# Kernel tuning notes

Hardware: AMD Instinct MI355X
Metric: run time of the kernel (lower is better)

The kernel has to match this reference:

```python
import jax, jax.numpy as jnp
import numpy as np

B, T, S, H, NH, F = 16, 512, 512, 1024, 16, 4096
HD = H // NH


def _mha(x, bias, mem, wq, bq, wk, bk, wv, bv, wo, bo):
    # THUMT MultiHeadAttention: q scaled by head_dim**-0.5, additive bias on logits
    b, t, h = x.shape
    q = (x @ wq + bq) * (HD ** -0.5)
    k = mem @ wk + bk
    v = mem @ wv + bv
    split = lambda z: z.reshape(z.shape[0], z.shape[1], NH, HD).transpose(0, 2, 1, 3)
    logits = jnp.einsum('bhqd,bhkd->bhqk', split(q), split(k)) + bias
    w = jax.nn.softmax(logits, axis=-1)
    o = jnp.einsum('bhqk,bhkd->bhqd', w, split(v))
    o = o.transpose(0, 2, 1, 3).reshape(b, t, h)
    return o @ wo + bo


def _lstm(inp, w, b):
    # inp: [B, T, 2H]; gates affine over concat([x_t, h], -1): [3H] -> [4H]
    bsz = inp.shape[0]
    def step(carry, xt):
        c, hdd = carry
        g = jnp.concatenate([xt, hdd], axis=-1) @ w + b
        i, j, f, o = jnp.split(g, 4, axis=-1)
        new_c = jax.nn.sigmoid(f) * c + jax.nn.sigmoid(i) * jnp.tanh(j)
        new_h = jax.nn.sigmoid(o) * jnp.tanh(new_c)
        return (new_c, new_h), new_h
    init = (jnp.zeros((bsz, H), inp.dtype), jnp.zeros((bsz, H), inp.dtype))
    _, hs = jax.lax.scan(step, init, inp.transpose(1, 0, 2))  # [T,B,H]
    return hs.transpose(1, 0, 2)


def setup_inputs() -> dict:
    key = jax.random.key(0)
    ks = jax.random.split(key, 16)
    d = {}
    d['x'] = jax.random.normal(ks[0], (B, T, H), jnp.float32)
    d['memory'] = jax.random.normal(ks[1], (B, S, H), jnp.float32)
    d['src_bias'] = jnp.zeros((B, 1, 1, S), jnp.float32)
    causal = jnp.triu(jnp.full((T, T), -1e9, jnp.float32), k=1)
    d['tgt_bias'] = causal[None, None]
    sc = 0.02
    names = ['src_wq', 'src_wk', 'src_wv', 'src_wo', 'tgt_wq', 'tgt_wk', 'tgt_wv', 'tgt_wo']
    for i, n in enumerate(names):
        d[n] = jax.random.normal(ks[2 + i], (H, H), jnp.float32) * sc
        d[n.replace('w', 'b')] = jnp.zeros((H,), jnp.float32)
    d['lstm_w'] = jax.random.normal(ks[10], (3 * H, 4 * H), jnp.float32) * sc
    d['lstm_b'] = jnp.zeros((4 * H,), jnp.float32)
    d['ffn_w1'] = jax.random.normal(ks[11], (H, F), jnp.float32) * sc
    d['ffn_b1'] = jnp.zeros((F,), jnp.float32)
    d['ffn_w2'] = jax.random.normal(ks[12], (F, H), jnp.float32) * sc
    d['ffn_b2'] = jnp.zeros((H,), jnp.float32)
    return d


def reference(x, memory, src_bias, tgt_bias,
              src_wq, src_bq, src_wk, src_bk, src_wv, src_bv, src_wo, src_bo,
              tgt_wq, tgt_bq, tgt_wk, tgt_bk, tgt_wv, tgt_bv, tgt_wo, tgt_bo,
              lstm_w, lstm_b, ffn_w1, ffn_b1, ffn_w2, ffn_b2):
    c_src = _mha(x, src_bias, memory, src_wq, src_bq, src_wk, src_bk, src_wv, src_bv, src_wo, src_bo)
    c_tgt = _mha(x, tgt_bias, x, tgt_wq, tgt_bq, tgt_wk, tgt_bk, tgt_wv, tgt_bv, tgt_wo, tgt_bo)
    c = c_src + c_tgt  # comb_mode='sum'
    hiddens = _lstm(jnp.concatenate([x, c], axis=-1), lstm_w, lstm_b)
    hiddens = jax.nn.relu(hiddens @ ffn_w1 + ffn_b1) @ ffn_w2 + ffn_b2  # FeedForward
    return hiddens  # dropout is identity in eval
```

## Files before the change

### kernel.cpp

```cpp
#include <hip/hip_runtime.h>
#include <hip/hip_bf16.h>
#include <stdint.h>


typedef unsigned short u16;
typedef unsigned int u32;
typedef unsigned long long u64;
typedef __bf16 bf16x8 __attribute__((ext_vector_type(8)));
typedef float f32x4 __attribute__((ext_vector_type(4)));
typedef int int32x4 __attribute__((ext_vector_type(4)));
typedef unsigned long long u64x2 __attribute__((ext_vector_type(2)));

#define DEV static __device__ __forceinline__

DEV u16 f2bf(float x) {
  u32 u = __builtin_bit_cast(u32, x);
  u += 0x7FFF + ((u >> 16) & 1);
  return (u16)(u >> 16);
}

DEV bf16x8 ldfrag(const void* p) {
  int32x4 v = *(const int32x4*)p;
  return __builtin_bit_cast(bf16x8, v);
}

DEV bf16x8 mkfrag(u64 lo, u64 hi) {
  u64x2 v;
  v.x = lo;
  v.y = hi;
  return __builtin_bit_cast(bf16x8, v);
}

DEV f32x4 mfma_bf16(bf16x8 a, bf16x8 b, f32x4 c) {
  return __builtin_amdgcn_mfma_f32_16x16x32_bf16(a, b, c, 0, 0, 0);
}

DEV void load_lds16(const u16* g, u16* l) {
  __builtin_amdgcn_global_load_lds(
      (__attribute__((address_space(1))) void*)(uintptr_t)g,
      (__attribute__((address_space(3))) void*)(uintptr_t)l, 16, 0, 0);
}


__global__ __launch_bounds__(256) void cvt_bf16_kernel(u16* __restrict__ out,
                                                       const float* __restrict__ in,
                                                       int n4) {
  int i = blockIdx.x * 256 + threadIdx.x;
  if (i >= n4) return;
  float4 v = ((const float4*)in)[i];
  ushort4 s;
  s.x = f2bf(v.x); s.y = f2bf(v.y); s.z = f2bf(v.z); s.w = f2bf(v.w);
  ((ushort4*)out)[i] = s;
}

__global__ __launch_bounds__(256) void cvt_x_kernel(u16* __restrict__ out,
                                                    const float* __restrict__ in) {
  int i = blockIdx.x * 256 + threadIdx.x;
  int r = i >> 8, cg4 = i & 255;
  float4 v = ((const float4*)in)[i];
  ushort4 s;
  s.x = f2bf(v.x); s.y = f2bf(v.y); s.z = f2bf(v.z); s.w = f2bf(v.w);
  *(ushort4*)(out + (size_t)r * 2048 + cg4 * 4) = s;
}

__global__ __launch_bounds__(256) void convt_kernel(u16* __restrict__ out,
                                                    const float* __restrict__ in,
                                                    int K, int N, int koff, float scale) {
  __shared__ float tile[32][33];
  const int tid = threadIdx.x;
  const int n0 = blockIdx.x * 32, k0 = blockIdx.y * 32;
  const int c = tid & 31, r = tid >> 5;
#pragma unroll
  for (int i = 0; i < 4; ++i)
    tile[r + i * 8][c] = in[(size_t)(k0 + r + i * 8 + koff) * N + n0 + c];
  __syncthreads();
#pragma unroll
  for (int i = 0; i < 4; ++i)
    out[(size_t)(n0 + r + i * 8) * K + k0 + c] = f2bf(tile[c][r + i * 8] * scale);
}

__global__ __launch_bounds__(256) void convt_perm_kernel(u16* __restrict__ out,
                                                         const float* __restrict__ in,
                                                         int K, int koff) {
  __shared__ float tile[32][33];
  const int tid = threadIdx.x;
  const int u0 = blockIdx.x * 32, k0 = blockIdx.y * 32, g = blockIdx.z;
  const int c = tid & 31, r = tid >> 5;
#pragma unroll
  for (int i = 0; i < 4; ++i)
    tile[r + i * 8][c] = in[(size_t)(k0 + r + i * 8 + koff) * 4096 + g * 1024 + u0 + c];
  __syncthreads();
#pragma unroll
  for (int i = 0; i < 4; ++i)
    out[(size_t)((u0 + r + i * 8) * 4 + g) * K + k0 + c] = f2bf(tile[c][r + i * 8]);
}

__global__ __launch_bounds__(256) void pack_bias_kernel(float* __restrict__ out,
                                                        const float* __restrict__ in) {
  int p = blockIdx.x * 256 + threadIdx.x;
  out[p] = in[(p & 3) * 1024 + (p >> 2)];
}

template <int OUTBF, int ACCUM, int RELU, int PERM>
__global__ __launch_bounds__(256) void gemm_bt_kernel(
    const u16* __restrict__ A, int lda, const u16* __restrict__ Bt,
    const float* __restrict__ bias, float bscale,
    void* __restrict__ outp, int ostride,
    const float* __restrict__ cacc, int cstride, int K) {
  __shared__ u16 As[128 * 32];
  __shared__ u16 Bs[128 * 32];
  const int tid = threadIdx.x;
  const int wave = tid >> 6, lane = tid & 63;
  const int lr = lane & 15, lg = lane >> 4;
  const int m0 = blockIdx.y * 128, n0 = blockIdx.x * 128;
  const int wr = (wave >> 1) * 64, wc = (wave & 1) * 64;

  f32x4 acc[4][4] = {};

  const int sr = lane >> 2, sce = (lane & 3) * 8;
  const u16* gA = A + (size_t)(m0 + wave * 16 + sr) * lda + sce;
  const u16* gB = Bt + (size_t)(n0 + wave * 16 + sr) * K + sce;
  u16* lA = As + wave * 16 * 32;
  u16* lB = Bs + wave * 16 * 32;

  for (int k0 = 0; k0 < K; k0 += 32) {
    __syncthreads();
    load_lds16(gA + k0, lA);
    load_lds16(gA + k0 + (size_t)64 * lda, lA + 64 * 32);
    load_lds16(gB + k0, lB);
    load_lds16(gB + k0 + (size_t)64 * K, lB + 64 * 32);
    __syncthreads();
    bf16x8 af[4], bfr[4];
    const u16* pa = As + (wr + lr) * 32 + lg * 8;
    const u16* pb = Bs + (wc + lr) * 32 + lg * 8;
#pragma unroll
    for (int i = 0; i < 4; ++i) af[i] = ldfrag(pa + i * 16 * 32);
#pragma unroll
    for (int j = 0; j < 4; ++j) bfr[j] = ldfrag(pb + j * 16 * 32);
#pragma unroll
    for (int i = 0; i < 4; ++i)
#pragma unroll
      for (int j = 0; j < 4; ++j)
        acc[i][j] = mfma_bf16(af[i], bfr[j], acc[i][j]);
  }

  const int col0 = n0 + wc + lr;
  const int row0 = m0 + wr + lg * 4;
#pragma unroll
  for (int i = 0; i < 4; ++i) {
#pragma unroll
    for (int j = 0; j < 4; ++j) {
      const int c = col0 + j * 16;
      const float bv = bias ? bias[c] * bscale : 0.f;
#pragma unroll
      for (int ii = 0; ii < 4; ++ii) {
        const int r = row0 + i * 16 + ii;
        float v = acc[i][j][ii] + bv;
        if (ACCUM) v += cacc[(size_t)r * cstride + c];
        if (RELU) v = fmaxf(v, 0.f);
        const int rp = (PERM == 2) ? ((r & 15) * 512 + (r >> 4)) : r;
        if (OUTBF) ((u16*)outp)[(size_t)rp * ostride + c] = f2bf(v);
        else       ((float*)outp)[(size_t)rp * ostride + c] = v;
      }
    }
  }
}

template <int CAUSAL>
__global__ __launch_bounds__(256) void flash_kernel(
    const u16* __restrict__ Q, const u16* __restrict__ Kb, const u16* __restrict__ Vb,
    const float* __restrict__ sbias, u16* __restrict__ O) {
  __shared__ u16 Kl[64 * 72];
  __shared__ u16 Vt[64 * 72];
  __shared__ u16 Pl[64 * 72];
  const int tid = threadIdx.x, wave = tid >> 6, lane = tid & 63;
  const int lr = lane & 15, lg = lane >> 4;
  const int q0 = blockIdx.x * 64, hh = blockIdx.y, b = blockIdx.z;

  bf16x8 qf[2];
  {
    const u16* qp = Q + (size_t)(b * 512 + q0 + wave * 16 + lr) * 1024 + hh * 64 + lg * 8;
    qf[0] = ldfrag(qp);
    qf[1] = ldfrag(qp + 32);
  }
  f32x4 oacc[4] = {};
  float mrun[4], lsum[4];
#pragma unroll
  for (int ii = 0; ii < 4; ++ii) { mrun[ii] = -3e38f; lsum[ii] = 0.f; }

  const int ntiles = CAUSAL ? (q0 / 64 + 1) : 8;
  for (int ti = 0; ti < ntiles; ++ti) {
    const int s0 = ti * 64;
    {
      const int r = tid >> 2, ch = (tid & 3) * 16;
      const u16* kp = Kb + (size_t)(b * 512 + s0 + r) * 1024 + hh * 64 + ch;
      const u16* vp = Vb + (size_t)(b * 512 + s0 + r) * 1024 + hh * 64 + ch;
      int32x4 k0v = *(const int32x4*)kp;
      int32x4 k1v = *(const int32x4*)(kp + 8);
      int32x4 v0v = *(const int32x4*)vp;
      int32x4 v1v = *(const int32x4*)(vp + 8);
      *(int32x4*)&Kl[r * 72 + ch] = k0v;
      *(int32x4*)&Kl[r * 72 + ch + 8] = k1v;
      const u16* v0p = (const u16*)&v0v;
      const u16* v1p = (const u16*)&v1v;
#pragma unroll
      for (int j = 0; j < 8; ++j) {
        Vt[(ch + j) * 72 + r] = v0p[j];
        Vt[(ch + 8 + j) * 72 + r] = v1p[j];
      }
    }
    __syncthreads();
    f32x4 sf[4] = {};
#pragma unroll
    for (int j = 0; j < 4; ++j)
#pragma unroll
      for (int ks = 0; ks < 2; ++ks) {
        bf16x8 kf = ldfrag(&Kl[(j * 16 + lr) * 72 + ks * 32 + lg * 8]);
        sf[j] = mfma_bf16(qf[ks], kf, sf[j]);
      }
    if (!CAUSAL) {
#pragma unroll
      for (int j = 0; j < 4; ++j) {
        const float bv = sbias[b * 512 + s0 + j * 16 + lr];
#pragma unroll
        for (int ii = 0; ii < 4; ++ii) sf[j][ii] += bv;
      }
    } else {
#pragma unroll
      for (int j = 0; j < 4; ++j) {
        const int s = s0 + j * 16 + lr;
#pragma unroll
        for (int ii = 0; ii < 4; ++ii) {
          const int q = q0 + wave * 16 + lg * 4 + ii;
          if (s > q) sf[j][ii] -= 1e9f;
        }
      }
    }
    float sc[4], rs[4];
#pragma unroll
    for (int ii = 0; ii < 4; ++ii) {
      float m = fmaxf(fmaxf(sf[0][ii], sf[1][ii]), fmaxf(sf[2][ii], sf[3][ii]));
#pragma unroll
      for (int off = 1; off < 16; off <<= 1) m = fmaxf(m, __shfl_xor(m, off));
      const float mn = fmaxf(mrun[ii], m);
      sc[ii] = __expf(mrun[ii] - mn);
      mrun[ii] = mn;
      rs[ii] = 0.f;
    }
#pragma unroll
    for (int j = 0; j < 4; ++j)
#pragma unroll
      for (int ii = 0; ii < 4; ++ii) {
        const float p = __expf(sf[j][ii] - mrun[ii]);
        rs[ii] += p;
        Pl[(wave * 16 + lg * 4 + ii) * 72 + j * 16 + lr] = f2bf(p);
      }
#pragma unroll
    for (int ii = 0; ii < 4; ++ii) {
      float r = rs[ii];
#pragma unroll
      for (int off = 1; off < 16; off <<= 1) r += __shfl_xor(r, off);
      lsum[ii] = lsum[ii] * sc[ii] + r;
    }
#pragma unroll
    for (int df = 0; df < 4; ++df)
#pragma unroll
      for (int ii = 0; ii < 4; ++ii) oacc[df][ii] *= sc[ii];
    __syncthreads();
    bf16x8 pf[2];
    pf[0] = ldfrag(&Pl[(wave * 16 + lr) * 72 + lg * 8]);
    pf[1] = ldfrag(&Pl[(wave * 16 + lr) * 72 + 32 + lg * 8]);
#pragma unroll
    for (int df = 0; df < 4; ++df)
#pragma unroll
      for (int ks = 0; ks < 2; ++ks) {
        bf16x8 vf = ldfrag(&Vt[(df * 16 + lr) * 72 + ks * 32 + lg * 8]);
        oacc[df] = mfma_bf16(pf[ks], vf, oacc[df]);
      }
    __syncthreads();
  }
#pragma unroll
  for (int df = 0; df < 4; ++df)
#pragma unroll
    for (int ii = 0; ii < 4; ++ii) {
      const float v = oacc[df][ii] / lsum[ii];
      O[(size_t)(b * 512 + q0 + wave * 16 + lg * 4 + ii) * 1024 + hh * 64 + df * 16 + lr] =
          f2bf(v);
    }
}

#define SCAN_NW 32
__global__ __launch_bounds__(256, 1) void lstm_scan_kernel(
    const u16* __restrict__ Whp, const float* __restrict__ gx,
    u16* __restrict__ hbuf) {
  const int tid = threadIdx.x, wave = tid >> 6, lane = tid & 63;
  const int lr = lane & 15, lg = lane >> 4;
  const int g = blockIdx.x;
  __shared__ float part[2][4][16][128];
  const int gb = tid >> 4;
  const int up = tid & 15;
  float cs0 = 0.f, cs1 = 0.f;
  const u64 SENT = 0xFFFFFFFFFFFFFFFFull;

  const u16* wbase = Whp + (size_t)(g * 128 + lr) * 1024 + wave * 256 + lg * 8;
  const float* gxp = gx + (size_t)gb * 512 * 4096 + g * 128 + up * 8;

  for (int t = 0; t < 512; ++t) {
    const float4 gxv0 = *(const float4*)(gxp + (size_t)t * 4096);
    const float4 gxv1 = *(const float4*)(gxp + (size_t)t * 4096 + 4);
    const u16* hp = hbuf + (size_t)t * 16384 + lr * 1024 + wave * 256 + lg * 8;
    u64 hw[16];
#pragma unroll
    for (int kc = 0; kc < 8; ++kc) {
      hw[kc * 2] = __hip_atomic_load((const u64*)(hp + kc * 32),
                                     __ATOMIC_RELAXED, __HIP_MEMORY_SCOPE_AGENT);
      hw[kc * 2 + 1] = __hip_atomic_load((const u64*)(hp + kc * 32 + 4),
                                         __ATOMIC_RELAXED, __HIP_MEMORY_SCOPE_AGENT);
    }
    {
      int guard = 0;
      for (;;) {
        bool ok = true;
#pragma unroll
        for (int i = 0; i < 16; ++i) ok &= (hw[i] != SENT);
        if (__all((int)ok)) break;
        __builtin_amdgcn_s_sleep(4);
        if (++guard > (1 << 20)) break;
#pragma unroll
        for (int kc = 0; kc < 8; ++kc) {
          if (hw[kc * 2] == SENT)
            hw[kc * 2] = __hip_atomic_load((const u64*)(hp + kc * 32),
                                           __ATOMIC_RELAXED, __HIP_MEMORY_SCOPE_AGENT);
          if (hw[kc * 2 + 1] == SENT)
            hw[kc * 2 + 1] = __hip_atomic_load((const u64*)(hp + kc * 32 + 4),
                                               __ATOMIC_RELAXED, __HIP_MEMORY_SCOPE_AGENT);
        }
      }
    }
    f32x4 acc[8] = {};
#pragma unroll
    for (int kc = 0; kc < 8; ++kc) {
      const bf16x8 hf = mkfrag(hw[kc * 2], hw[kc * 2 + 1]);
#pragma unroll
      for (int j = 0; j < 8; ++j)
        acc[j] = mfma_bf16(hf, ldfrag(wbase + j * 16 * 1024 + kc * 32), acc[j]);
    }
    const int p = t & 1;
#pragma unroll
    for (int j = 0; j < 8; ++j)
#pragma unroll
      for (int ii = 0; ii < 4; ++ii)
        part[p][wave][lg * 4 + ii][j * 16 + lr] = acc[j][ii];
    __syncthreads();
    float s[8];
#pragma unroll
    for (int k = 0; k < 8; ++k)
      s[k] = part[p][0][gb][up * 8 + k] + part[p][1][gb][up * 8 + k] +
             part[p][2][gb][up * 8 + k] + part[p][3][gb][up * 8 + k];
    float hA, hB;
    {
      const float si = s[0] + gxv0.x, sj = s[1] + gxv0.y;
      const float sf_ = s[2] + gxv0.z, so = s[3] + gxv0.w;
      const float ig = 1.f / (1.f + __expf(-si));
      const float jg = 1.f - 2.f / (__expf(2.f * sj) + 1.f);
      const float fg = 1.f / (1.f + __expf(-sf_));
      const float og = 1.f / (1.f + __expf(-so));
      cs0 = fg * cs0 + ig * jg;
      hA = og * (1.f - 2.f / (__expf(2.f * cs0) + 1.f));
    }
    {
      const float si = s[4] + gxv1.x, sj = s[5] + gxv1.y;
      const float sf_ = s[6] + gxv1.z, so = s[7] + gxv1.w;
      const float ig = 1.f / (1.f + __expf(-si));
      const float jg = 1.f - 2.f / (__expf(2.f * sj) + 1.f);
      const float fg = 1.f / (1.f + __expf(-sf_));
      const float og = 1.f / (1.f + __expf(-so));
      cs1 = fg * cs1 + ig * jg;
      hB = og * (1.f - 2.f / (__expf(2.f * cs1) + 1.f));
    }
    const u32 myw = (u32)f2bf(hA) | ((u32)f2bf(hB) << 16);
    const u32 otherw = (u32)__shfl_down((int)myw, 1);
    if (!(up & 1)) {
      u64 w64 = (u64)myw | ((u64)otherw << 32);
      u64* dst = (u64*)(hbuf + (size_t)(t + 1) * 16384 + gb * 1024 + g * 32 + up * 2);
      __hip_atomic_store(dst, w64, __ATOMIC_RELAXED, __HIP_MEMORY_SCOPE_AGENT);
    }
  }
}


extern "C" void kernel_launch(void* const* d_in, const int* in_sizes, int n_in,
                              void* d_out, int out_size, void* d_ws, size_t ws_size,
                              hipStream_t stream) {
  const float* x        = (const float*)d_in[0];
  const float* mem      = (const float*)d_in[1];
  const float* src_bias = (const float*)d_in[2];
  const float* w_src_q = (const float*)d_in[4];  const float* b_src_q = (const float*)d_in[5];
  const float* w_src_k = (const float*)d_in[6];  const float* b_src_k = (const float*)d_in[7];
  const float* w_src_v = (const float*)d_in[8];  const float* b_src_v = (const float*)d_in[9];
  const float* w_src_o = (const float*)d_in[10]; const float* b_src_o = (const float*)d_in[11];
  const float* w_tgt_q = (const float*)d_in[12]; const float* b_tgt_q = (const float*)d_in[13];
  const float* w_tgt_k = (const float*)d_in[14]; const float* b_tgt_k = (const float*)d_in[15];
  const float* w_tgt_v = (const float*)d_in[16]; const float* b_tgt_v = (const float*)d_in[17];
  const float* w_tgt_o = (const float*)d_in[18]; const float* b_tgt_o = (const float*)d_in[19];
  const float* lstm_w  = (const float*)d_in[20]; const float* lstm_b  = (const float*)d_in[21];
  const float* w1 = (const float*)d_in[22]; const float* b1f = (const float*)d_in[23];
  const float* w2 = (const float*)d_in[24]; const float* b2f = (const float*)d_in[25];

  char* ws = (char*)d_ws;
  const size_t MiB = 1024ull * 1024ull;
  u16*   xcb  = (u16*)(ws + 0);
  u16*   wlp  = (u16*)(ws + 32 * MiB);
  u16*   whp  = (u16*)(ws + 48 * MiB);
  u16*   w1t  = (u16*)(ws + 56 * MiB);
  u16*   w2t  = (u16*)(ws + 64 * MiB);
  float* pb   = (float*)(ws + 72 * MiB);
  u16*   hbuf = (u16*)(ws + 73 * MiB);
  u16*   memb = (u16*)(ws + 90 * MiB);
  u16*   wt[8];
  for (int i = 0; i < 8; ++i) wt[i] = (u16*)(ws + 106 * MiB + (size_t)i * 2 * MiB);
  u16*   bq   = (u16*)(ws + 122 * MiB);
  u16*   bk   = (u16*)(ws + 138 * MiB);
  u16*   bv   = (u16*)(ws + 154 * MiB);
  u16*   ao_s = (u16*)(ws + 170 * MiB);
  u16*   ao_t = (u16*)(ws + 186 * MiB);
  float* c32  = (float*)(ws + 202 * MiB);
  float* gx   = (float*)(ws + 90 * MiB);
  u16*   ffn1 = (u16*)(ws + 90 * MiB);

  hipMemsetAsync(hbuf + 16384, 0xFF, (size_t)512 * 16384 * 2, stream);
  hipMemsetAsync(hbuf, 0, 32768, stream);

  cvt_x_kernel<<<8192, 256, 0, stream>>>(xcb, x);
  cvt_bf16_kernel<<<8192, 256, 0, stream>>>(memb, mem, 2097152);
  const dim3 g1k(32, 32);
  convt_kernel<<<g1k, 256, 0, stream>>>(wt[0], w_src_q, 1024, 1024, 0, 0.125f);
  convt_kernel<<<g1k, 256, 0, stream>>>(wt[1], w_src_k, 1024, 1024, 0, 1.f);
  convt_kernel<<<g1k, 256, 0, stream>>>(wt[2], w_src_v, 1024, 1024, 0, 1.f);
  convt_kernel<<<g1k, 256, 0, stream>>>(wt[3], w_src_o, 1024, 1024, 0, 1.f);
  convt_kernel<<<g1k, 256, 0, stream>>>(wt[4], w_tgt_q, 1024, 1024, 0, 0.125f);
  convt_kernel<<<g1k, 256, 0, stream>>>(wt[5], w_tgt_k, 1024, 1024, 0, 1.f);
  convt_kernel<<<g1k, 256, 0, stream>>>(wt[6], w_tgt_v, 1024, 1024, 0, 1.f);
  convt_kernel<<<g1k, 256, 0, stream>>>(wt[7], w_tgt_o, 1024, 1024, 0, 1.f);
  convt_perm_kernel<<<dim3(32, 64, 4), 256, 0, stream>>>(wlp, lstm_w, 2048, 0);
  convt_perm_kernel<<<dim3(32, 32, 4), 256, 0, stream>>>(whp, lstm_w, 1024, 2048);
  convt_kernel<<<dim3(128, 32), 256, 0, stream>>>(w1t, w1, 1024, 4096, 0, 1.f);
  convt_kernel<<<dim3(32, 128), 256, 0, stream>>>(w2t, w2, 4096, 1024, 0, 1.f);
  pack_bias_kernel<<<16, 256, 0, stream>>>(pb, lstm_b);

  const dim3 gN1(8, 64);
  const dim3 gN4(32, 64);

  gemm_bt_kernel<1, 0, 0, 0><<<gN1, 256, 0, stream>>>(xcb, 2048, wt[0], b_src_q, 0.125f, bq, 1024, nullptr, 0, 1024);
  gemm_bt_kernel<1, 0, 0, 0><<<gN1, 256, 0, stream>>>(memb, 1024, wt[1], b_src_k, 1.f, bk, 1024, nullptr, 0, 1024);
  gemm_bt_kernel<1, 0, 0, 0><<<gN1, 256, 0, stream>>>(memb, 1024, wt[2], b_src_v, 1.f, bv, 1024, nullptr, 0, 1024);
  flash_kernel<0><<<dim3(8, 16, 16), 256, 0, stream>>>(bq, bk, bv, src_bias, ao_s);
  gemm_bt_kernel<1, 0, 0, 0><<<gN1, 256, 0, stream>>>(xcb, 2048, wt[4], b_tgt_q, 0.125f, bq, 1024, nullptr, 0, 1024);
  gemm_bt_kernel<1, 0, 0, 0><<<gN1, 256, 0, stream>>>(xcb, 2048, wt[5], b_tgt_k, 1.f, bk, 1024, nullptr, 0, 1024);
  gemm_bt_kernel<1, 0, 0, 0><<<gN1, 256, 0, stream>>>(xcb, 2048, wt[6], b_tgt_v, 1.f, bv, 1024, nullptr, 0, 1024);
  flash_kernel<1><<<dim3(8, 16, 16), 256, 0, stream>>>(bq, bk, bv, nullptr, ao_t);
  gemm_bt_kernel<0, 0, 0, 0><<<gN1, 256, 0, stream>>>(ao_s, 1024, wt[3], b_src_o, 1.f, c32, 1024, nullptr, 0, 1024);
  gemm_bt_kernel<1, 1, 0, 0><<<gN1, 256, 0, stream>>>(ao_t, 1024, wt[7], b_tgt_o, 1.f, xcb + 1024, 2048, c32, 1024, 1024);
  gemm_bt_kernel<0, 0, 0, 0><<<gN4, 256, 0, stream>>>(xcb, 2048, wlp, pb, 1.f, gx, 4096, nullptr, 0, 2048);
  lstm_scan_kernel<<<dim3(SCAN_NW), 256, 0, stream>>>(whp, gx, hbuf);
  gemm_bt_kernel<1, 0, 1, 0><<<gN4, 256, 0, stream>>>(hbuf + 16384, 1024, w1t, b1f, 1.f, ffn1, 4096, nullptr, 0, 1024);
  gemm_bt_kernel<0, 0, 0, 2><<<gN1, 256, 0, stream>>>(ffn1, 4096, w2t, b2f, 1.f, (float*)d_out, 1024, nullptr, 0, 4096);
}
```

Before: 3.002 ms.

## Fuse QKV projection GEMMs, swizzle GEMM tile order, pad LSTM LDS partials

Merges the separate target Q/K/V projection GEMMs into one wide GEMM producing an interleaved [rows, 3072] buffer. It does the same for the source K/V pair into [rows, 2048], using the fact that the transposed weights sit back to back in the workspace. Biases are packed by a new small kernel, and the flash kernel takes row strides so it can read the interleaved buffers. It also remaps workgroup IDs in the GEMM so tiles sharing operands run together, and pads the LSTM scan's shared partial-sum array to cut bank conflicts. The aim is fewer launches, better operand reuse and fewer LDS conflicts. The risk is that the fused GEMM depends on the implicit contiguous weight layout.

```diff
diff --git a/kernel.cpp b/kernel.cpp
--- a/kernel.cpp
+++ b/kernel.cpp
@@ -33,6 +33,10 @@
 
 DEV f32x4 mfma_bf16(bf16x8 a, bf16x8 b, f32x4 c) {
   return __builtin_amdgcn_mfma_f32_16x16x32_bf16(a, b, c, 0, 0, 0);
+}
+
+DEV u64 aload(const u64* p) {
+  return __hip_atomic_load(p, __ATOMIC_RELAXED, __HIP_MEMORY_SCOPE_AGENT);
 }
 
 DEV void load_lds16(const u16* g, u16* l) {
@@ -99,6 +103,14 @@
                                                         const float* __restrict__ in) {
   int p = blockIdx.x * 256 + threadIdx.x;
   out[p] = in[(p & 3) * 1024 + (p >> 2)];
+}
+
+__global__ __launch_bounds__(256) void pack_bias3_kernel(
+    float* __restrict__ out, const float* __restrict__ b0,
+    const float* __restrict__ b1, const float* __restrict__ b2, float s0) {
+  int p = blockIdx.x * 256 + threadIdx.x;
+  float v = (p < 1024) ? b0[p] * s0 : (p < 2048 ? b1[p - 1024] : b2[p - 2048]);
+  out[p] = v;
 }
 
 template <int OUTBF, int ACCUM, int RELU, int PERM>
@@ -112,7 +124,10 @@
   const int tid = threadIdx.x;
   const int wave = tid >> 6, lane = tid & 63;
   const int lr = lane & 15, lg = lane >> 4;
-  const int m0 = blockIdx.y * 128, n0 = blockIdx.x * 128;
+  const int nwg = gridDim.x * gridDim.y;
+  const int wgid = blockIdx.y * gridDim.x + blockIdx.x;
+  const int swz = (wgid & 7) * (nwg >> 3) + (wgid >> 3);
+  const int m0 = (swz / gridDim.x) * 128, n0 = (swz % gridDim.x) * 128;
   const int wr = (wave >> 1) * 64, wc = (wave & 1) * 64;
 
   f32x4 acc[4][4] = {};
@@ -169,7 +184,7 @@
 template <int CAUSAL>
 __global__ __launch_bounds__(256) void flash_kernel(
     const u16* __restrict__ Q, const u16* __restrict__ Kb, const u16* __restrict__ Vb,
-    const float* __restrict__ sbias, u16* __restrict__ O) {
+    const float* __restrict__ sbias, u16* __restrict__ O, int qs, int ks) {
   __shared__ u16 Kl[64 * 72];
   __shared__ u16 Vt[64 * 72];
   __shared__ u16 Pl[64 * 72];
@@ -179,7 +194,7 @@
 
   bf16x8 qf[2];
   {
-    const u16* qp = Q + (size_t)(b * 512 + q0 + wave * 16 + lr) * 1024 + hh * 64 + lg * 8;
+    const u16* qp = Q + (size_t)(b * 512 + q0 + wave * 16 + lr) * qs + hh * 64 + lg * 8;
     qf[0] = ldfrag(qp);
     qf[1] = ldfrag(qp + 32);
   }
@@ -193,8 +208,8 @@
     const int s0 = ti * 64;
     {
       const int r = tid >> 2, ch = (tid & 3) * 16;
-      const u16* kp = Kb + (size_t)(b * 512 + s0 + r) * 1024 + hh * 64 + ch;
-      const u16* vp = Vb + (size_t)(b * 512 + s0 + r) * 1024 + hh * 64 + ch;
+      const u16* kp = Kb + (size_t)(b * 512 + s0 + r) * ks + hh * 64 + ch;
+      const u16* vp = Vb + (size_t)(b * 512 + s0 + r) * ks + hh * 64 + ch;
       int32x4 k0v = *(const int32x4*)kp;
       int32x4 k1v = *(const int32x4*)(kp + 8);
       int32x4 v0v = *(const int32x4*)vp;
@@ -214,9 +229,9 @@
 #pragma unroll
     for (int j = 0; j < 4; ++j)
 #pragma unroll
-      for (int ks = 0; ks < 2; ++ks) {
-        bf16x8 kf = ldfrag(&Kl[(j * 16 + lr) * 72 + ks * 32 + lg * 8]);
-        sf[j] = mfma_bf16(qf[ks], kf, sf[j]);
+      for (int ks2 = 0; ks2 < 2; ++ks2) {
+        bf16x8 kf = ldfrag(&Kl[(j * 16 + lr) * 72 + ks2 * 32 + lg * 8]);
+        sf[j] = mfma_bf16(qf[ks2], kf, sf[j]);
       }
     if (!CAUSAL) {
 #pragma unroll
@@ -273,9 +288,9 @@
 #pragma unroll
     for (int df = 0; df < 4; ++df)
 #pragma unroll
-      for (int ks = 0; ks < 2; ++ks) {
-        bf16x8 vf = ldfrag(&Vt[(df * 16 + lr) * 72 + ks * 32 + lg * 8]);
-        oacc[df] = mfma_bf16(pf[ks], vf, oacc[df]);
+      for (int ks2 = 0; ks2 < 2; ++ks2) {
+        bf16x8 vf = ldfrag(&Vt[(df * 16 + lr) * 72 + ks2 * 32 + lg * 8]);
+        oacc[df] = mfma_bf16(pf[ks2], vf, oacc[df]);
       }
     __syncthreads();
   }
@@ -296,7 +311,7 @@
   const int tid = threadIdx.x, wave = tid >> 6, lane = tid & 63;
   const int lr = lane & 15, lg = lane >> 4;
   const int g = blockIdx.x;
-  __shared__ float part[2][4][16][128];
+  __shared__ float part[2][4][16][132];
   const int gb = tid >> 4;
   const int up = tid & 15;
   float cs0 = 0.f, cs1 = 0.f;
@@ -304,18 +319,17 @@
 
   const u16* wbase = Whp + (size_t)(g * 128 + lr) * 1024 + wave * 256 + lg * 8;
   const float* gxp = gx + (size_t)gb * 512 * 4096 + g * 128 + up * 8;
+  const size_t goff = (size_t)lr * 1024 + wave * 256 + lg * 8;
 
   for (int t = 0; t < 512; ++t) {
     const float4 gxv0 = *(const float4*)(gxp + (size_t)t * 4096);
     const float4 gxv1 = *(const float4*)(gxp + (size_t)t * 4096 + 4);
-    const u16* hp = hbuf + (size_t)t * 16384 + lr * 1024 + wave * 256 + lg * 8;
+    const u16* hp = hbuf + (size_t)t * 16384 + goff;
     u64 hw[16];
 #pragma unroll
     for (int kc = 0; kc < 8; ++kc) {
-      hw[kc * 2] = __hip_atomic_load((const u64*)(hp + kc * 32),
-                                     __ATOMIC_RELAXED, __HIP_MEMORY_SCOPE_AGENT);
-      hw[kc * 2 + 1] = __hip_atomic_load((const u64*)(hp + kc * 32 + 4),
-                                         __ATOMIC_RELAXED, __HIP_MEMORY_SCOPE_AGENT);
+      hw[kc * 2] = aload((const u64*)(hp + kc * 32));
+      hw[kc * 2 + 1] = aload((const u64*)(hp + kc * 32 + 4));
     }
     {
       int guard = 0;
@@ -329,11 +343,9 @@
 #pragma unroll
         for (int kc = 0; kc < 8; ++kc) {
           if (hw[kc * 2] == SENT)
-            hw[kc * 2] = __hip_atomic_load((const u64*)(hp + kc * 32),
-                                           __ATOMIC_RELAXED, __HIP_MEMORY_SCOPE_AGENT);
+            hw[kc * 2] = aload((const u64*)(hp + kc * 32));
           if (hw[kc * 2 + 1] == SENT)
-            hw[kc * 2 + 1] = __hip_atomic_load((const u64*)(hp + kc * 32 + 4),
-                                               __ATOMIC_RELAXED, __HIP_MEMORY_SCOPE_AGENT);
+            hw[kc * 2 + 1] = aload((const u64*)(hp + kc * 32 + 4));
         }
       }
     }
@@ -382,7 +394,8 @@
     const u32 otherw = (u32)__shfl_down((int)myw, 1);
     if (!(up & 1)) {
       u64 w64 = (u64)myw | ((u64)otherw << 32);
-      u64* dst = (u64*)(hbuf + (size_t)(t + 1) * 16384 + gb * 1024 + g * 32 + up * 2);
+      u64* dst = (u64*)(hbuf + (size_t)(t + 1) * 16384 + (size_t)gb * 1024 +
+                        g * 32 + up * 2);
       __hip_atomic_store(dst, w64, __ATOMIC_RELAXED, __HIP_MEMORY_SCOPE_AGENT);
     }
   }
@@ -415,13 +428,15 @@
   u16*   w1t  = (u16*)(ws + 56 * MiB);
   u16*   w2t  = (u16*)(ws + 64 * MiB);
   float* pb   = (float*)(ws + 72 * MiB);
+  float* pb3  = pb + 4096;
+  float* pb2  = pb3 + 3072;
   u16*   hbuf = (u16*)(ws + 73 * MiB);
   u16*   memb = (u16*)(ws + 90 * MiB);
   u16*   wt[8];
   for (int i = 0; i < 8; ++i) wt[i] = (u16*)(ws + 106 * MiB + (size_t)i * 2 * MiB);
-  u16*   bq   = (u16*)(ws + 122 * MiB);
-  u16*   bk   = (u16*)(ws + 138 * MiB);
-  u16*   bv   = (u16*)(ws + 154 * MiB);
+  u16*   qsrc = (u16*)(ws + 122 * MiB);
+  u16*   kvs  = (u16*)(ws + 138 * MiB);
+  u16*   qkv  = (u16*)(ws + 122 * MiB);
   u16*   ao_s = (u16*)(ws + 170 * MiB);
   u16*   ao_t = (u16*)(ws + 186 * MiB);
   float* c32  = (float*)(ws + 202 * MiB);
@@ -447,22 +462,18 @@
   convt_kernel<<<dim3(128, 32), 256, 0, stream>>>(w1t, w1, 1024, 4096, 0, 1.f);
   convt_kernel<<<dim3(32, 128), 256, 0, stream>>>(w2t, w2, 4096, 1024, 0, 1.f);
   pack_bias_kernel<<<16, 256, 0, stream>>>(pb, lstm_b);
-
-  const dim3 gN1(8, 64);
-  const dim3 gN4(32, 64);
-
-  gemm_bt_kernel<1, 0, 0, 0><<<gN1, 256, 0, stream>>>(xcb, 2048, wt[0], b_src_q, 0.125f, bq, 1024, nullptr, 0, 1024);
-  gemm_bt_kernel<1, 0, 0, 0><<<gN1, 256, 0, stream>>>(memb, 1024, wt[1], b_src_k, 1.f, bk, 1024, nullptr, 0, 1024);
-  gemm_bt_kernel<1, 0, 0, 0><<<gN1, 256, 0, stream>>>(memb, 1024, wt[2], b_src_v, 1.f, bv, 1024, nullptr, 0, 1024);
-  flash_kernel<0><<<dim3(8, 16, 16), 256, 0, stream>>>(bq, bk, bv, src_bias, ao_s);
-  gemm_bt_kernel<1, 0, 0, 0><<<gN1, 256, 0, stream>>>(xcb, 2048, wt[4], b_tgt_q, 0.125f, bq, 1024, nullptr, 0, 1024);
-  gemm_bt_kernel<1, 0, 0, 0><<<gN1, 256, 0, stream>>>(xcb, 2048, wt[5], b_tgt_k, 1.f, bk, 1024, nullptr, 0, 1024);
-  gemm_bt_kernel<1, 0, 0, 0><<<gN1, 256, 0, stream>>>(xcb, 2048, wt[6], b_tgt_v, 1.f, bv, 1024, nullptr, 0, 1024);
-  flash_kernel<1><<<dim3(8, 16, 16), 256, 0, stream>>>(bq, bk, bv, nullptr, ao_t);
-  gemm_bt_kernel<0, 0, 0, 0><<<gN1, 256, 0, stream>>>(ao_s, 1024, wt[3], b_src_o, 1.f, c32, 1024, nullptr, 0, 1024);
-  gemm_bt_kernel<1, 1, 0, 0><<<gN1, 256, 0, stream>>>(ao_t, 1024, wt[7], b_tgt_o, 1.f, xcb + 1024, 2048, c32, 1024, 1024);
-  gemm_bt_kernel<0, 0, 0, 0><<<gN4, 256, 0, stream>>>(xcb, 2048, wlp, pb, 1.f, gx, 4096, nullptr, 0, 2048);
+  pack_bias3_kernel<<<12, 256, 0, stream>>>(pb3, b_tgt_q, b_tgt_k, b_tgt_v, 0.125f);
+  pack_bias3_kernel<<<8, 256, 0, stream>>>(pb2, b_src_k, b_src_v, b_src_v, 1.f);
+
+  gemm_bt_kernel<1, 0, 0, 0><<<dim3(8, 64), 256, 0, stream>>>(xcb, 2048, wt[0], b_src_q, 0.125f, qsrc, 1024, nullptr, 0, 1024);
+  gemm_bt_kernel<1, 0, 0, 0><<<dim3(16, 64), 256, 0, stream>>>(memb, 1024, wt[1], pb2, 1.f, kvs, 2048, nullptr, 0, 1024);
+  flash_kernel<0><<<dim3(8, 16, 16), 256, 0, stream>>>(qsrc, kvs, kvs + 1024, src_bias, ao_s, 1024, 2048);
+  gemm_bt_kernel<1, 0, 0, 0><<<dim3(24, 64), 256, 0, stream>>>(xcb, 2048, wt[4], pb3, 1.f, qkv, 3072, nullptr, 0, 1024);
+  flash_kernel<1><<<dim3(8, 16, 16), 256, 0, stream>>>(qkv, qkv + 1024, qkv + 2048, nullptr, ao_t, 3072, 3072);
+  gemm_bt_kernel<0, 0, 0, 0><<<dim3(8, 64), 256, 0, stream>>>(ao_s, 1024, wt[3], b_src_o, 1.f, c32, 1024, nullptr, 0, 1024);
+  gemm_bt_kernel<1, 1, 0, 0><<<dim3(8, 64), 256, 0, stream>>>(ao_t, 1024, wt[7], b_tgt_o, 1.f, xcb + 1024, 2048, c32, 1024, 1024);
+  gemm_bt_kernel<0, 0, 0, 0><<<dim3(32, 64), 256, 0, stream>>>(xcb, 2048, wlp, pb, 1.f, gx, 4096, nullptr, 0, 2048);
   lstm_scan_kernel<<<dim3(SCAN_NW), 256, 0, stream>>>(whp, gx, hbuf);
-  gemm_bt_kernel<1, 0, 1, 0><<<gN4, 256, 0, stream>>>(hbuf + 16384, 1024, w1t, b1f, 1.f, ffn1, 4096, nullptr, 0, 1024);
-  gemm_bt_kernel<0, 0, 0, 2><<<gN1, 256, 0, stream>>>(ffn1, 4096, w2t, b2f, 1.f, (float*)d_out, 1024, nullptr, 0, 4096);
-}
+  gemm_bt_kernel<1, 0, 1, 0><<<dim3(32, 64), 256, 0, stream>>>(hbuf + 16384, 1024, w1t, b1f, 1.f, ffn1, 4096, nullptr, 0, 1024);
+  gemm_bt_kernel<0, 0, 0, 2><<<dim3(8, 64), 256, 0, stream>>>(ffn1, 4096, w2t, b2f, 1.f, (float*)d_out, 1024, nullptr, 0, 4096);
+}
```

Measured after the change: 2.956 ms. About the same (-1.6%).
